# Optimization experiments

Measured on AMD Instinct MI355X. Metric: run time of the kernel, lower is better.

## Reference

```python
import jax, jax.numpy as jnp
import numpy as np
from functools import partial

# dims matching init_kwargs
H = 512      # hidden_size
F = 2048     # ff_size
NH = 8       # num_heads
NL = 6       # num_layers
V = 1024     # vocab_size
T = 8        # sentence_length
S = 5        # n_sentences_in_paragraph
P = 16       # n_paragraphs_in_article
L = P * S * T          # article_length = 640
N = L + 1              # sequence length used by masks = 641
B = 16                 # batch
HD = H // NH           # head dim
LN_EPS = 1e-5
NEG = -1e9


def _build_mask():
    # pseudo_causal_masks[0] from the torch __init__: causal ~tril plus
    # blocking of within-paragraph sentence-0 key columns.
    a = np.ones((P, S, T, P, S, T), dtype=bool)
    j = np.arange(P)
    a[j, :, :, j, 0, :] = False
    a = a.reshape(L, L)
    causal = ~np.tril(np.ones((N, N), dtype=bool))
    m = causal.copy()
    m[:-1, 1:] = np.logical_and(a, causal[:-1, 1:])
    return m  # True = disallowed


def _build_pe():
    # sinusoidal pe exactly as in __init__ (div_term uses hidden_size in denom)
    pos = np.arange(N, dtype=np.float32)[:, None]
    div = np.exp(np.arange(0, H // 2, dtype=np.float32) * (-np.log(10000.0) / H))
    pe = np.zeros((N, H), dtype=np.float32)
    pe[:, 0::2] = np.sin(pos * div)
    pe[:, 1::2] = np.cos(pos * div)
    return pe


def setup_inputs() -> dict:
    key = jax.random.key(0)
    ks = jax.random.split(key, 12)
    sd = 0.02
    inp = {
        'tokens': jax.random.randint(ks[0], (B, N), 0, V),
        'attn_mask': jnp.asarray(_build_mask()),
        'pe': jnp.asarray(_build_pe()),
        'emb': jax.random.normal(ks[1], (V, H), jnp.float32) * sd,
        'qkv_w': jax.random.normal(ks[2], (NL, 3 * H, H), jnp.float32) * sd,
        'qkv_b': jnp.zeros((NL, 3 * H), jnp.float32),
        'out_w': jax.random.normal(ks[3], (NL, H, H), jnp.float32) * sd,
        'out_b': jnp.zeros((NL, H), jnp.float32),
        'ln1_g': jnp.ones((NL, H), jnp.float32),
        'ln1_b': jnp.zeros((NL, H), jnp.float32),
        'fc1_w': jax.random.normal(ks[4], (NL, F, H), jnp.float32) * sd,
        'fc1_b': jnp.zeros((NL, F), jnp.float32),
        'fc2_w': jax.random.normal(ks[5], (NL, H, F), jnp.float32) * sd,
        'fc2_b': jnp.zeros((NL, H), jnp.float32),
        'ln2_g': jnp.ones((NL, H), jnp.float32),
        'ln2_b': jnp.zeros((NL, H), jnp.float32),
        'lnf_g': jnp.ones((H,), jnp.float32),
        'lnf_b': jnp.zeros((H,), jnp.float32),
        'dep_w': jax.random.normal(ks[6], (V, H), jnp.float32) * sd,
        'dep_b': jnp.zeros((V,), jnp.float32),
    }
    return inp


def _ln(x, g, b):
    m = jnp.mean(x, axis=-1, keepdims=True)
    v = jnp.mean(jnp.square(x - m), axis=-1, keepdims=True)
    return (x - m) * jax.lax.rsqrt(v + LN_EPS) * g + b


def _encoder_layer(x, p, mask):
    qw, qb, ow, ob, g1, b1, w1, bb1, w2, bb2, g2, b2 = p
    Bsz, Nn, _ = x.shape
    qkv = x @ qw.T + qb                                   # [B,N,3H]
    q, k, v = jnp.split(qkv, 3, axis=-1)
    q = q.reshape(Bsz, Nn, NH, HD)
    k = k.reshape(Bsz, Nn, NH, HD)
    v = v.reshape(Bsz, Nn, NH, HD)
    scores = jnp.einsum('bqhd,bkhd->bhqk', q, k) / jnp.sqrt(jnp.asarray(HD, x.dtype))
    scores = jnp.where(mask[None, None], NEG, scores)
    att = jax.nn.softmax(scores, axis=-1)
    o = jnp.einsum('bhqk,bkhd->bqhd', att, v).reshape(Bsz, Nn, H)
    o = o @ ow.T + ob
    x = _ln(x + o, g1, b1)                                # post-LN (torch default)
    f = jax.nn.gelu(x @ w1.T + bb1, approximate=False) @ w2.T + bb2
    return _ln(x + f, g2, b2)


def reference(tokens, attn_mask, pe, emb, qkv_w, qkv_b, out_w, out_b,
              ln1_g, ln1_b, fc1_w, fc1_b, fc2_w, fc2_b, ln2_g, ln2_b,
              lnf_g, lnf_b, dep_w, dep_b):
    x = emb[tokens] + pe[None]                            # [B,N,H]
    layers = (qkv_w, qkv_b, out_w, out_b, ln1_g, ln1_b,
              fc1_w, fc1_b, fc2_w, fc2_b, ln2_g, ln2_b)

    def step(h, p):
        return _encoder_layer(h, p, attn_mask), None

    x, _ = jax.lax.scan(step, x, layers)
    x = _ln(x, lnf_g, lnf_b)
    return x @ dep_w.T + dep_b                            # [B,N,V] logits
```

## Files before the change

### kernel.cpp

```cpp
#include <hip/hip_runtime.h>
#include <stdint.h>

#define NSEQ 641
#define BATCH 16
#define MROWS (BATCH * NSEQ)
#define HID 512
#define FFD 2048
#define NHEAD 8
#define HDIM 64
#define NLAYER 6
#define VOCAB 1024
#define KPAD 704

typedef __bf16 bf16x8 __attribute__((ext_vector_type(8)));
typedef float  f32x4  __attribute__((ext_vector_type(4)));
typedef int    i32x4  __attribute__((ext_vector_type(4)));
typedef short  s16x8  __attribute__((ext_vector_type(8)));
typedef short  s16x4  __attribute__((ext_vector_type(4)));

__device__ __forceinline__ uint32_t swz(uint32_t b) { return b ^ (((b >> 7) & 7u) << 4); }

__device__ __forceinline__ unsigned short f2bf(float f) {
  uint32_t u = __builtin_bit_cast(uint32_t, f);
  u += 0x7FFFu + ((u >> 16) & 1u);
  return (unsigned short)(u >> 16);
}

__device__ __forceinline__ void gload16(const void* g, void* l) {
  __builtin_amdgcn_global_load_lds(
      (const __attribute__((address_space(1))) uint32_t*)g,
      (__attribute__((address_space(3))) uint32_t*)l, 16, 0, 0);
}

__device__ __forceinline__ bf16x8 ld_lds16(const void* p) {
  return __builtin_bit_cast(bf16x8, *(const i32x4*)p);
}

__global__ void cvt_kernel(const float* __restrict__ in,
                           unsigned short* __restrict__ out, int n) {
  int i = (blockIdx.x * 256 + threadIdx.x) * 4;
  if (i >= n) return;
  f32x4 v = *(const f32x4*)(in + i);
  s16x4 o;
  o[0] = (short)f2bf(v[0]); o[1] = (short)f2bf(v[1]);
  o[2] = (short)f2bf(v[2]); o[3] = (short)f2bf(v[3]);
  *(s16x4*)(out + i) = o;
}

__global__ void embed_kernel(const int* __restrict__ tok,
                             const float* __restrict__ emb,
                             const float* __restrict__ pe,
                             float* __restrict__ x,
                             unsigned short* __restrict__ xb) {
  int m = blockIdx.x;
  int n = m % NSEQ;
  int t = tok[m];
  int h = threadIdx.x * 4;
  f32x4 e = *(const f32x4*)(emb + (size_t)t * HID + h);
  f32x4 p = *(const f32x4*)(pe + (size_t)n * HID + h);
  f32x4 v = e + p;
  *(f32x4*)(x + (size_t)m * HID + h) = v;
  s16x4 o;
  o[0] = (short)f2bf(v[0]); o[1] = (short)f2bf(v[1]);
  o[2] = (short)f2bf(v[2]); o[3] = (short)f2bf(v[3]);
  *(s16x4*)(xb + (size_t)m * HID + h) = o;
}

__global__ __launch_bounds__(256) void ln_kernel(
    const float* __restrict__ in, const float* __restrict__ gg,
    const float* __restrict__ bb, float* __restrict__ xo,
    unsigned short* __restrict__ xbo, int rows) {
  int row = blockIdx.x * 4 + (threadIdx.x >> 6);
  if (row >= rows) return;
  int lane = threadIdx.x & 63;
  const float* p = in + (size_t)row * HID + lane * 8;
  f32x4 a0 = *(const f32x4*)p;
  f32x4 a1 = *(const f32x4*)(p + 4);
  float s = a0[0] + a0[1] + a0[2] + a0[3] + a1[0] + a1[1] + a1[2] + a1[3];
#pragma unroll
  for (int o = 32; o; o >>= 1) s += __shfl_xor(s, o);
  float mean = s * (1.0f / HID);
  float vs = 0.f;
#pragma unroll
  for (int j = 0; j < 4; ++j) { float d = a0[j] - mean; vs += d * d; }
#pragma unroll
  for (int j = 0; j < 4; ++j) { float d = a1[j] - mean; vs += d * d; }
#pragma unroll
  for (int o = 32; o; o >>= 1) vs += __shfl_xor(vs, o);
  float rstd = rsqrtf(vs * (1.0f / HID) + 1e-5f);
  f32x4 g0 = *(const f32x4*)(gg + lane * 8);
  f32x4 g1 = *(const f32x4*)(gg + lane * 8 + 4);
  f32x4 b0 = *(const f32x4*)(bb + lane * 8);
  f32x4 b1 = *(const f32x4*)(bb + lane * 8 + 4);
  f32x4 y0, y1;
  s16x8 ob;
#pragma unroll
  for (int j = 0; j < 4; ++j) {
    y0[j] = (a0[j] - mean) * rstd * g0[j] + b0[j];
    y1[j] = (a1[j] - mean) * rstd * g1[j] + b1[j];
    ob[j] = (short)f2bf(y0[j]);
    ob[j + 4] = (short)f2bf(y1[j]);
  }
  float* xp = xo + (size_t)row * HID + lane * 8;
  *(f32x4*)xp = y0;
  *(f32x4*)(xp + 4) = y1;
  *(s16x8*)(xbo + (size_t)row * HID + lane * 8) = ob;
}

__global__ __launch_bounds__(256) void vtrans_kernel(
    const unsigned short* __restrict__ V, unsigned short* __restrict__ vT) {
  const int kt = blockIdx.x;
  const int bh = blockIdx.y;
  const int k0 = kt * 64;
  const int tid = threadIdx.x;
  __shared__ unsigned short lds[64][68];
  const size_t src = (size_t)bh * (NSEQ * HDIM);
#pragma unroll
  for (int it = 0; it < 2; ++it) {
    int k = it * 32 + (tid >> 3);
    int d0 = (tid & 7) * 8;
    int kr = k0 + k;
    s16x8 v = {};
    if (kr < NSEQ) v = *(const s16x8*)(V + src + (size_t)kr * HDIM + d0);
    *(s16x8*)&lds[k][d0] = v;
  }
  __syncthreads();
  const int d = tid & 63;
  const int w = tid >> 6;
  const size_t dst = ((size_t)bh * 64 + d) * KPAD + k0;
#pragma unroll
  for (int it = 0; it < 2; ++it) {
    int kc = w + it * 4;
    s16x8 o;
#pragma unroll
    for (int i = 0; i < 8; ++i) o[i] = lds[kc * 8 + i][d];
    *(s16x8*)(vT + dst + kc * 8) = o;
  }
}

enum { EPI_QKV = 0, EPI_GELU = 1, EPI_RESID = 2, EPI_F32OUT = 3 };

template <int EPI>
__global__ __launch_bounds__(256, 2) void gemm_bt(
    const unsigned short* __restrict__ A, const unsigned short* __restrict__ W,
    const float* __restrict__ bias, const float* __restrict__ resid,
    void* __restrict__ out0, void* __restrict__ out1, void* __restrict__ out2,
    int M, int N, int K) {
  __shared__ char sm[32768];
  const int tid = threadIdx.x, lane = tid & 63, wid = tid >> 6;
  const int wr = wid >> 1, wc = wid & 1;
  const int m0 = blockIdx.y * 128, n0 = blockIdx.x * 128;
  f32x4 acc[4][4] = {};
  const uint32_t Pbase = wid * 4096;

  for (int kt = 0; kt < K; kt += 64) {
#pragma unroll
    for (int i = 0; i < 4; ++i) {
      uint32_t P = Pbase + i * 1024 + lane * 16;
      uint32_t L = swz(P);
      int row = (int)(L >> 7);
      uint32_t kb = L & 127u;
      int ma = m0 + row; if (ma >= M) ma = M - 1;
      gload16((const char*)A + ((size_t)ma * K + kt) * 2 + kb, sm + Pbase + i * 1024);
      gload16((const char*)W + ((size_t)(n0 + row) * K + kt) * 2 + kb,
              sm + 16384 + Pbase + i * 1024);
    }
    __syncthreads();
#pragma unroll
    for (int kk = 0; kk < 2; ++kk) {
      bf16x8 af[4], bfr[4];
#pragma unroll
      for (int mi = 0; mi < 4; ++mi) {
        int row = wr * 64 + mi * 16 + (lane & 15);
        af[mi] = ld_lds16(sm + swz((uint32_t)row * 128 + kk * 64 + ((lane >> 4) << 4)));
      }
#pragma unroll
      for (int ni = 0; ni < 4; ++ni) {
        int row = wc * 64 + ni * 16 + (lane & 15);
        bfr[ni] = ld_lds16(sm + 16384 + swz((uint32_t)row * 128 + kk * 64 + ((lane >> 4) << 4)));
      }
#pragma unroll
      for (int mi = 0; mi < 4; ++mi)
#pragma unroll
        for (int ni = 0; ni < 4; ++ni)
          acc[mi][ni] = __builtin_amdgcn_mfma_f32_16x16x32_bf16(af[mi], bfr[ni], acc[mi][ni], 0, 0, 0);
    }
    __syncthreads();
  }

#pragma unroll
  for (int mi = 0; mi < 4; ++mi) {
#pragma unroll
    for (int g = 0; g < 4; ++g) {
      int m = m0 + wr * 64 + mi * 16 + (lane >> 4) * 4 + g;
      if (m >= M) continue;
      int bbq = 0, nn = 0;
      if (EPI == EPI_QKV) { bbq = m / NSEQ; nn = m - bbq * NSEQ; }
#pragma unroll
      for (int ni = 0; ni < 4; ++ni) {
        int c = n0 + wc * 64 + ni * 16 + (lane & 15);
        float v = acc[mi][ni][g] + bias[c];
        if (EPI == EPI_QKV) {
          int which = c >> 9, hh = (c >> 6) & 7, d = c & 63;
          unsigned short* dst = which == 0 ? (unsigned short*)out0
                              : which == 1 ? (unsigned short*)out1
                                           : (unsigned short*)out2;
          dst[(((size_t)bbq * NHEAD + hh) * NSEQ + nn) * HDIM + d] = f2bf(v);
        } else if (EPI == EPI_GELU) {
          v = 0.5f * v * (1.0f + erff(v * 0.70710678118654752f));
          ((unsigned short*)out0)[(size_t)m * N + c] = f2bf(v);
        } else if (EPI == EPI_RESID) {
          float* o = (float*)out0;
          o[(size_t)m * N + c] = v + resid[(size_t)m * N + c];
        } else {
          ((float*)out0)[(size_t)m * N + c] = v;
        }
      }
    }
  }
}

__global__ __launch_bounds__(256) void attn_kernel(
    const unsigned short* __restrict__ Q, const unsigned short* __restrict__ Kb,
    const unsigned short* __restrict__ vT, unsigned short* __restrict__ O) {
  const int qt = blockIdx.x, bh = blockIdx.y;
  const int b = bh >> 3, h = bh & 7;
  const int q0 = qt * 64;
  const int tid = threadIdx.x, lane = tid & 63, w = tid >> 6;
  const int lg = lane >> 4, lc = lane & 15;
  __shared__ char sK[8192];
  __shared__ char sV[8192];
  __shared__ char sP[4][2048];

  const size_t base = (size_t)bh * (NSEQ * HDIM);
  const size_t baseT = (size_t)bh * (HDIM * KPAD);

  bf16x8 qf[2];
  {
    int qr = q0 + w * 16 + lc;
    if (qr > NSEQ - 1) qr = NSEQ - 1;
#pragma unroll
    for (int kk = 0; kk < 2; ++kk)
      qf[kk] = __builtin_bit_cast(
          bf16x8, *(const i32x4*)(Q + base + (size_t)qr * HDIM + kk * 32 + (lg << 3)));
  }

  f32x4 acc[4] = {};
  float mrow[4] = {-1e30f, -1e30f, -1e30f, -1e30f};
  float lrow[4] = {0.f, 0.f, 0.f, 0.f};
  const int qrow_base = q0 + w * 16 + (lg << 2);

  int nkt = (q0 + 103) / 64 + 1;
  if (nkt > 11) nkt = 11;

  for (int kt = 0; kt < nkt; ++kt) {
    const int k0 = kt * 64;
#pragma unroll
    for (int i = 0; i < 2; ++i) {
      uint32_t P = w * 2048 + i * 1024 + lane * 16;
      uint32_t L = swz(P);
      int row = (int)(L >> 7);
      uint32_t kbyte = L & 127u;
      int kr = k0 + row; if (kr > NSEQ - 1) kr = NSEQ - 1;
      gload16((const char*)(Kb + base + (size_t)kr * HDIM) + kbyte, sK + w * 2048 + i * 1024);
    }
#pragma unroll
    for (int i = 0; i < 2; ++i) {
      uint32_t P = w * 2048 + i * 1024 + lane * 16;
      uint32_t L = swz(P);
      int drow = (int)(L >> 7);
      uint32_t kbyte = L & 127u;
      gload16((const char*)(vT + baseT + (size_t)drow * KPAD + k0) + kbyte,
              sV + w * 2048 + i * 1024);
    }
    __syncthreads();

    f32x4 s[4] = {};
#pragma unroll
    for (int nt = 0; nt < 4; ++nt) {
#pragma unroll
      for (int kk = 0; kk < 2; ++kk) {
        int row = nt * 16 + lc;
        bf16x8 kf = ld_lds16(sK + swz((uint32_t)row * 128 + kk * 64 + (lg << 4)));
        s[nt] = __builtin_amdgcn_mfma_f32_16x16x32_bf16(qf[kk], kf, s[nt], 0, 0, 0);
      }
    }
    float mx[4];
#pragma unroll
    for (int g = 0; g < 4; ++g) {
      int q = qrow_base + g;
      int p = q / 40;
      int lo = p * 40 + 1, hi = p * 40 + 8;
      float best = -1e30f;
#pragma unroll
      for (int nt = 0; nt < 4; ++nt) {
        int k = k0 + nt * 16 + lc;
        bool ok = ((k <= q) || (k >= lo && k <= hi)) && (k < NSEQ);
        float v = ok ? s[nt][g] * 0.125f : -1e30f;
        s[nt][g] = v;
        best = fmaxf(best, v);
      }
      mx[g] = best;
    }
#pragma unroll
    for (int o = 1; o < 16; o <<= 1)
#pragma unroll
      for (int g = 0; g < 4; ++g) mx[g] = fmaxf(mx[g], __shfl_xor(mx[g], o));

    float alpha[4], rs[4];
#pragma unroll
    for (int g = 0; g < 4; ++g) {
      float mnew = fmaxf(mrow[g], mx[g]);
      alpha[g] = __expf(mrow[g] - mnew);
      mrow[g] = mnew;
      float sum = 0.f;
#pragma unroll
      for (int nt = 0; nt < 4; ++nt) {
        float pv = __expf(s[nt][g] - mnew);
        s[nt][g] = pv;
        sum += pv;
      }
      rs[g] = sum;
    }
#pragma unroll
    for (int o = 1; o < 16; o <<= 1)
#pragma unroll
      for (int g = 0; g < 4; ++g) rs[g] += __shfl_xor(rs[g], o);
#pragma unroll
    for (int g = 0; g < 4; ++g) {
      lrow[g] = lrow[g] * alpha[g] + rs[g];
#pragma unroll
      for (int nt = 0; nt < 4; ++nt) acc[nt][g] *= alpha[g];
    }

#pragma unroll
    for (int g = 0; g < 4; ++g) {
      int row = (lg << 2) + g;
#pragma unroll
      for (int nt = 0; nt < 4; ++nt) {
        int col = nt * 16 + lc;
        *(short*)(sP[w] + swz((uint32_t)row * 128 + col * 2)) = (short)f2bf(s[nt][g]);
      }
    }
#pragma unroll
    for (int kk = 0; kk < 2; ++kk) {
      bf16x8 pa = ld_lds16(sP[w] + swz((uint32_t)lc * 128 + kk * 64 + (lg << 4)));
#pragma unroll
      for (int nt = 0; nt < 4; ++nt) {
        int rowv = nt * 16 + lc;
        bf16x8 vf = ld_lds16(sV + swz((uint32_t)rowv * 128 + kk * 64 + (lg << 4)));
        acc[nt] = __builtin_amdgcn_mfma_f32_16x16x32_bf16(pa, vf, acc[nt], 0, 0, 0);
      }
    }
    __syncthreads();
  }

#pragma unroll
  for (int g = 0; g < 4; ++g) {
    int q = qrow_base + g;
    if (q >= NSEQ) continue;
    float inv = 1.0f / lrow[g];
#pragma unroll
    for (int nt = 0; nt < 4; ++nt) {
      int d = nt * 16 + lc;
      O[((size_t)b * NSEQ + q) * HID + h * HDIM + d] = f2bf(acc[nt][g] * inv);
    }
  }
}

extern "C" void kernel_launch(void* const* d_in, const int* in_sizes, int n_in,
                              void* d_out, int out_size, void* d_ws, size_t ws_size,
                              hipStream_t stream) {
  const int*   tok   = (const int*)d_in[0];
  const float* pe    = (const float*)d_in[2];
  const float* emb   = (const float*)d_in[3];
  const float* qkv_w = (const float*)d_in[4];
  const float* qkv_b = (const float*)d_in[5];
  const float* out_w = (const float*)d_in[6];
  const float* out_b = (const float*)d_in[7];
  const float* ln1_g = (const float*)d_in[8];
  const float* ln1_b = (const float*)d_in[9];
  const float* fc1_w = (const float*)d_in[10];
  const float* fc1_b = (const float*)d_in[11];
  const float* fc2_w = (const float*)d_in[12];
  const float* fc2_b = (const float*)d_in[13];
  const float* ln2_g = (const float*)d_in[14];
  const float* ln2_b = (const float*)d_in[15];
  const float* lnf_g = (const float*)d_in[16];
  const float* lnf_b = (const float*)d_in[17];
  const float* dep_w = (const float*)d_in[18];
  const float* dep_b = (const float*)d_in[19];

  const size_t SZ_QKV = (size_t)1536 * 512;
  const size_t SZ_OUT = (size_t)512 * 512;
  const size_t SZ_FC1 = (size_t)2048 * 512;
  const size_t SZ_FC2 = (size_t)512 * 2048;
  const size_t SZ_DEP = (size_t)VOCAB * 512;

  char* w = (char*)d_ws;
  float* x = (float*)w;            w += (size_t)MROWS * HID * 4;
  unsigned short* xb = (unsigned short*)w; w += (size_t)MROWS * HID * 2;
  unsigned short* qb = (unsigned short*)w; w += (size_t)BATCH * NHEAD * NSEQ * HDIM * 2;
  unsigned short* kb = (unsigned short*)w; w += (size_t)BATCH * NHEAD * NSEQ * HDIM * 2;
  unsigned short* vb = (unsigned short*)w; w += (size_t)BATCH * NHEAD * NSEQ * HDIM * 2;
  unsigned short* ao = (unsigned short*)w; w += (size_t)BATCH * NHEAD * NSEQ * HDIM * 2;
  unsigned short* mid = qb;
  unsigned short* vT = (unsigned short*)w; w += (size_t)BATCH * NHEAD * HDIM * KPAD * 2;

  size_t used = (size_t)(w - (char*)d_ws);
  size_t all_w_bytes = (NLAYER * (SZ_QKV + SZ_OUT + SZ_FC1 + SZ_FC2) + SZ_DEP) * 2;
  bool upfront = ws_size >= used + all_w_bytes;

  unsigned short *wq_all, *wo_all, *w1_all, *w2_all, *wd;
  if (upfront) {
    wq_all = (unsigned short*)w; w += NLAYER * SZ_QKV * 2;
    wo_all = (unsigned short*)w; w += NLAYER * SZ_OUT * 2;
    w1_all = (unsigned short*)w; w += NLAYER * SZ_FC1 * 2;
    w2_all = (unsigned short*)w; w += NLAYER * SZ_FC2 * 2;
    wd     = (unsigned short*)w; w += SZ_DEP * 2;
    cvt_kernel<<<dim3((NLAYER * SZ_QKV) / 1024), 256, 0, stream>>>(qkv_w, wq_all, NLAYER * SZ_QKV);
    cvt_kernel<<<dim3((NLAYER * SZ_OUT) / 1024), 256, 0, stream>>>(out_w, wo_all, NLAYER * SZ_OUT);
    cvt_kernel<<<dim3((NLAYER * SZ_FC1) / 1024), 256, 0, stream>>>(fc1_w, w1_all, NLAYER * SZ_FC1);
    cvt_kernel<<<dim3((NLAYER * SZ_FC2) / 1024), 256, 0, stream>>>(fc2_w, w2_all, NLAYER * SZ_FC2);
    cvt_kernel<<<dim3(SZ_DEP / 1024), 256, 0, stream>>>(dep_w, wd, SZ_DEP);
  } else {
    wq_all = (unsigned short*)w; w += SZ_QKV * 2;
    wo_all = (unsigned short*)w; w += SZ_OUT * 2;
    w1_all = (unsigned short*)w; w += SZ_FC1 * 2;
    w2_all = (unsigned short*)w; w += SZ_FC2 * 2;
    wd     = (unsigned short*)w; w += SZ_DEP * 2;
    cvt_kernel<<<dim3(SZ_DEP / 1024), 256, 0, stream>>>(dep_w, wd, SZ_DEP);
  }

  embed_kernel<<<dim3(MROWS), 128, 0, stream>>>(tok, emb, pe, x, xb);

  const int lnBlocks = (MROWS + 3) / 4;
  for (int l = 0; l < NLAYER; ++l) {
    unsigned short *wq, *wo, *w1, *w2;
    if (upfront) {
      wq = wq_all + l * SZ_QKV; wo = wo_all + l * SZ_OUT;
      w1 = w1_all + l * SZ_FC1; w2 = w2_all + l * SZ_FC2;
    } else {
      wq = wq_all; wo = wo_all; w1 = w1_all; w2 = w2_all;
      cvt_kernel<<<dim3(SZ_QKV / 1024), 256, 0, stream>>>(qkv_w + l * SZ_QKV, wq, SZ_QKV);
      cvt_kernel<<<dim3(SZ_OUT / 1024), 256, 0, stream>>>(out_w + l * SZ_OUT, wo, SZ_OUT);
      cvt_kernel<<<dim3(SZ_FC1 / 1024), 256, 0, stream>>>(fc1_w + l * SZ_FC1, w1, SZ_FC1);
      cvt_kernel<<<dim3(SZ_FC2 / 1024), 256, 0, stream>>>(fc2_w + l * SZ_FC2, w2, SZ_FC2);
    }

    gemm_bt<EPI_QKV><<<dim3(12, 81), 256, 0, stream>>>(
        xb, wq, qkv_b + l * 1536, nullptr, qb, kb, vb, MROWS, 1536, 512);
    vtrans_kernel<<<dim3(11, 128), 256, 0, stream>>>(vb, vT);
    attn_kernel<<<dim3(11, 128), 256, 0, stream>>>(qb, kb, vT, ao);
    gemm_bt<EPI_RESID><<<dim3(4, 81), 256, 0, stream>>>(
        ao, wo, out_b + l * 512, x, x, nullptr, nullptr, MROWS, 512, 512);
    ln_kernel<<<dim3(lnBlocks), 256, 0, stream>>>(x, ln1_g + l * 512, ln1_b + l * 512, x, xb, MROWS);
    gemm_bt<EPI_GELU><<<dim3(16, 81), 256, 0, stream>>>(
        xb, w1, fc1_b + l * 2048, nullptr, mid, nullptr, nullptr, MROWS, 2048, 512);
    gemm_bt<EPI_RESID><<<dim3(4, 81), 256, 0, stream>>>(
        mid, w2, fc2_b + l * 512, x, x, nullptr, nullptr, MROWS, 512, 2048);
    ln_kernel<<<dim3(lnBlocks), 256, 0, stream>>>(x, ln2_g + l * 512, ln2_b + l * 512, x, xb, MROWS);
  }

  ln_kernel<<<dim3(lnBlocks), 256, 0, stream>>>(x, lnf_g, lnf_b, x, xb, MROWS);
  gemm_bt<EPI_F32OUT><<<dim3(8, 81), 256, 0, stream>>>(
      xb, wd, dep_b, nullptr, d_out, nullptr, nullptr, MROWS, VOCAB, 512);
}
```

Measured before the change: 1.507 ms.

## Double-buffer GEMM and attention tiles, drop online-softmax max tracking

```diff
diff --git a/kernel.cpp b/kernel.cpp
--- a/kernel.cpp
+++ b/kernel.cpp
@@ -17,6 +17,8 @@
 typedef int    i32x4  __attribute__((ext_vector_type(4)));
 typedef short  s16x8  __attribute__((ext_vector_type(8)));
 typedef short  s16x4  __attribute__((ext_vector_type(4)));
+
+#define EXP_C 0.18033688011112042f
 
 __device__ __forceinline__ uint32_t swz(uint32_t b) { return b ^ (((b >> 7) & 7u) << 4); }
 
@@ -146,14 +148,14 @@
     const float* __restrict__ bias, const float* __restrict__ resid,
     void* __restrict__ out0, void* __restrict__ out1, void* __restrict__ out2,
     int M, int N, int K) {
-  __shared__ char sm[32768];
+  __shared__ char sm[2][32768];
   const int tid = threadIdx.x, lane = tid & 63, wid = tid >> 6;
   const int wr = wid >> 1, wc = wid & 1;
   const int m0 = blockIdx.y * 128, n0 = blockIdx.x * 128;
   f32x4 acc[4][4] = {};
   const uint32_t Pbase = wid * 4096;
 
-  for (int kt = 0; kt < K; kt += 64) {
+  auto stage = [&](int kt, char* dst) {
 #pragma unroll
     for (int i = 0; i < 4; ++i) {
       uint32_t P = Pbase + i * 1024 + lane * 16;
@@ -161,23 +163,31 @@
       int row = (int)(L >> 7);
       uint32_t kb = L & 127u;
       int ma = m0 + row; if (ma >= M) ma = M - 1;
-      gload16((const char*)A + ((size_t)ma * K + kt) * 2 + kb, sm + Pbase + i * 1024);
+      gload16((const char*)A + ((size_t)ma * K + kt) * 2 + kb, dst + Pbase + i * 1024);
       gload16((const char*)W + ((size_t)(n0 + row) * K + kt) * 2 + kb,
-              sm + 16384 + Pbase + i * 1024);
-    }
-    __syncthreads();
+              dst + 16384 + Pbase + i * 1024);
+    }
+  };
+
+  const int nk = K >> 6;
+  stage(0, sm[0]);
+  __syncthreads();
+
+  for (int t = 0; t < nk; ++t) {
+    if (t + 1 < nk) stage((t + 1) << 6, sm[(t + 1) & 1]);
+    const char* buf = sm[t & 1];
 #pragma unroll
     for (int kk = 0; kk < 2; ++kk) {
       bf16x8 af[4], bfr[4];
 #pragma unroll
       for (int mi = 0; mi < 4; ++mi) {
         int row = wr * 64 + mi * 16 + (lane & 15);
-        af[mi] = ld_lds16(sm + swz((uint32_t)row * 128 + kk * 64 + ((lane >> 4) << 4)));
+        af[mi] = ld_lds16(buf + swz((uint32_t)row * 128 + kk * 64 + ((lane >> 4) << 4)));
       }
 #pragma unroll
       for (int ni = 0; ni < 4; ++ni) {
         int row = wc * 64 + ni * 16 + (lane & 15);
-        bfr[ni] = ld_lds16(sm + 16384 + swz((uint32_t)row * 128 + kk * 64 + ((lane >> 4) << 4)));
+        bfr[ni] = ld_lds16(buf + 16384 + swz((uint32_t)row * 128 + kk * 64 + ((lane >> 4) << 4)));
       }
 #pragma unroll
       for (int mi = 0; mi < 4; ++mi)
@@ -228,8 +238,8 @@
   const int q0 = qt * 64;
   const int tid = threadIdx.x, lane = tid & 63, w = tid >> 6;
   const int lg = lane >> 4, lc = lane & 15;
-  __shared__ char sK[8192];
-  __shared__ char sV[8192];
+  __shared__ char sK[2][8192];
+  __shared__ char sV[2][8192];
   __shared__ char sP[4][2048];
 
   const size_t base = (size_t)bh * (NSEQ * HDIM);
@@ -246,14 +256,13 @@
   }
 
   f32x4 acc[4] = {};
-  float mrow[4] = {-1e30f, -1e30f, -1e30f, -1e30f};
-  float lrow[4] = {0.f, 0.f, 0.f, 0.f};
+  float lsum[4] = {0.f, 0.f, 0.f, 0.f};
   const int qrow_base = q0 + w * 16 + (lg << 2);
 
-  int nkt = (q0 + 103) / 64 + 1;
+  int nkt = qt + 2;
   if (nkt > 11) nkt = 11;
 
-  for (int kt = 0; kt < nkt; ++kt) {
+  auto stage = [&](int kt, int bufi) {
     const int k0 = kt * 64;
 #pragma unroll
     for (int i = 0; i < 2; ++i) {
@@ -262,18 +271,21 @@
       int row = (int)(L >> 7);
       uint32_t kbyte = L & 127u;
       int kr = k0 + row; if (kr > NSEQ - 1) kr = NSEQ - 1;
-      gload16((const char*)(Kb + base + (size_t)kr * HDIM) + kbyte, sK + w * 2048 + i * 1024);
-    }
-#pragma unroll
-    for (int i = 0; i < 2; ++i) {
-      uint32_t P = w * 2048 + i * 1024 + lane * 16;
-      uint32_t L = swz(P);
-      int drow = (int)(L >> 7);
-      uint32_t kbyte = L & 127u;
-      gload16((const char*)(vT + baseT + (size_t)drow * KPAD + k0) + kbyte,
-              sV + w * 2048 + i * 1024);
-    }
-    __syncthreads();
+      gload16((const char*)(Kb + base + (size_t)kr * HDIM) + kbyte,
+              sK[bufi] + w * 2048 + i * 1024);
+      gload16((const char*)(vT + baseT + (size_t)row * KPAD + k0) + kbyte,
+              sV[bufi] + w * 2048 + i * 1024);
+    }
+  };
+
+  stage(0, 0);
+  __syncthreads();
+
+  for (int kt = 0; kt < nkt; ++kt) {
+    if (kt + 1 < nkt) stage(kt + 1, (kt + 1) & 1);
+    const char* bK = sK[kt & 1];
+    const char* bV = sV[kt & 1];
+    const int k0 = kt * 64;
 
     f32x4 s[4] = {};
 #pragma unroll
@@ -281,56 +293,50 @@
 #pragma unroll
       for (int kk = 0; kk < 2; ++kk) {
         int row = nt * 16 + lc;
-        bf16x8 kf = ld_lds16(sK + swz((uint32_t)row * 128 + kk * 64 + (lg << 4)));
+        bf16x8 kf = ld_lds16(bK + swz((uint32_t)row * 128 + kk * 64 + (lg << 4)));
         s[nt] = __builtin_amdgcn_mfma_f32_16x16x32_bf16(qf[kk], kf, s[nt], 0, 0, 0);
       }
     }
-    float mx[4];
-#pragma unroll
-    for (int g = 0; g < 4; ++g) {
-      int q = qrow_base + g;
-      int p = q / 40;
-      int lo = p * 40 + 1, hi = p * 40 + 8;
-      float best = -1e30f;
-#pragma unroll
-      for (int nt = 0; nt < 4; ++nt) {
-        int k = k0 + nt * 16 + lc;
-        bool ok = ((k <= q) || (k >= lo && k <= hi)) && (k < NSEQ);
-        float v = ok ? s[nt][g] * 0.125f : -1e30f;
-        s[nt][g] = v;
-        best = fmaxf(best, v);
-      }
-      mx[g] = best;
-    }
-#pragma unroll
-    for (int o = 1; o < 16; o <<= 1)
-#pragma unroll
-      for (int g = 0; g < 4; ++g) mx[g] = fmaxf(mx[g], __shfl_xor(mx[g], o));
-
-    float alpha[4], rs[4];
-#pragma unroll
-    for (int g = 0; g < 4; ++g) {
-      float mnew = fmaxf(mrow[g], mx[g]);
-      alpha[g] = __expf(mrow[g] - mnew);
-      mrow[g] = mnew;
-      float sum = 0.f;
-#pragma unroll
-      for (int nt = 0; nt < 4; ++nt) {
-        float pv = __expf(s[nt][g] - mnew);
-        s[nt][g] = pv;
-        sum += pv;
-      }
-      rs[g] = sum;
-    }
-#pragma unroll
-    for (int o = 1; o < 16; o <<= 1)
-#pragma unroll
-      for (int g = 0; g < 4; ++g) rs[g] += __shfl_xor(rs[g], o);
-#pragma unroll
-    for (int g = 0; g < 4; ++g) {
-      lrow[g] = lrow[g] * alpha[g] + rs[g];
-#pragma unroll
-      for (int nt = 0; nt < 4; ++nt) acc[nt][g] *= alpha[g];
+
+    if (kt < qt) {
+#pragma unroll
+      for (int g = 0; g < 4; ++g)
+#pragma unroll
+        for (int nt = 0; nt < 4; ++nt) {
+          float p = exp2f(s[nt][g] * EXP_C);
+          s[nt][g] = p;
+          lsum[g] += p;
+        }
+    } else if (kt == qt) {
+#pragma unroll
+      for (int g = 0; g < 4; ++g) {
+        int q = qrow_base + g;
+        int pp = q / 40;
+        int lo = pp * 40 + 1, hi = pp * 40 + 8;
+#pragma unroll
+        for (int nt = 0; nt < 4; ++nt) {
+          int k = k0 + nt * 16 + lc;
+          bool ok = ((k <= q) || (k >= lo && k <= hi)) && (k < NSEQ);
+          float p = ok ? exp2f(s[nt][g] * EXP_C) : 0.f;
+          s[nt][g] = p;
+          lsum[g] += p;
+        }
+      }
+    } else {
+#pragma unroll
+      for (int g = 0; g < 4; ++g) {
+        int q = qrow_base + g;
+        int pp = q / 40;
+        int lo = pp * 40 + 1, hi = pp * 40 + 8;
+#pragma unroll
+        for (int nt = 0; nt < 4; ++nt) {
+          int k = k0 + nt * 16 + lc;
+          bool ok = (k >= lo && k <= hi) && (k < NSEQ);
+          float p = ok ? exp2f(s[nt][g] * EXP_C) : 0.f;
+          s[nt][g] = p;
+          lsum[g] += p;
+        }
+      }
     }
 
 #pragma unroll
@@ -348,18 +354,23 @@
 #pragma unroll
       for (int nt = 0; nt < 4; ++nt) {
         int rowv = nt * 16 + lc;
-        bf16x8 vf = ld_lds16(sV + swz((uint32_t)rowv * 128 + kk * 64 + (lg << 4)));
+        bf16x8 vf = ld_lds16(bV + swz((uint32_t)rowv * 128 + kk * 64 + (lg << 4)));
         acc[nt] = __builtin_amdgcn_mfma_f32_16x16x32_bf16(pa, vf, acc[nt], 0, 0, 0);
       }
     }
     __syncthreads();
   }
+
+#pragma unroll
+  for (int o = 1; o < 16; o <<= 1)
+#pragma unroll
+    for (int g = 0; g < 4; ++g) lsum[g] += __shfl_xor(lsum[g], o);
 
 #pragma unroll
   for (int g = 0; g < 4; ++g) {
     int q = qrow_base + g;
     if (q >= NSEQ) continue;
-    float inv = 1.0f / lrow[g];
+    float inv = 1.0f / lsum[g];
 #pragma unroll
     for (int nt = 0; nt < 4; ++nt) {
       int d = nt * 16 + lc;
```

New measurement: 1.393 ms. -7.5%, faster.
